# Optimization experiments

Measured on AMD Instinct MI355X. Metric: run time of the kernel, lower is better.

## Reference

```python
import jax, jax.numpy as jnp
import numpy as np
from math import sqrt

B, L, S = 8, 1024, 1000
D_MODEL, D_LLM, H, E = 1024, 4096, 16, 64  # d_keys = d_model // n_heads = 64


def setup_inputs() -> dict:
    key = jax.random.key(0)
    ks = jax.random.split(key, 11)
    s = 0.02
    return {
        "target_embedding": jax.random.normal(ks[0], (B, L, D_MODEL), jnp.float32),
        "source_embedding": jax.random.normal(ks[1], (S, D_LLM), jnp.float32),
        "value_embedding": jax.random.normal(ks[2], (S, D_LLM), jnp.float32),
        "Wq": jax.random.normal(ks[3], (D_MODEL, H * E), jnp.float32) * s,
        "bq": jnp.zeros((H * E,), jnp.float32),
        "Wk": jax.random.normal(ks[4], (D_LLM, H * E), jnp.float32) * s,
        "bk": jnp.zeros((H * E,), jnp.float32),
        "Wv": jax.random.normal(ks[5], (D_LLM, H * E), jnp.float32) * s,
        "bv": jnp.zeros((H * E,), jnp.float32),
        "Wo": jax.random.normal(ks[6], (H * E, D_LLM), jnp.float32) * s,
        "bo": jnp.zeros((D_LLM,), jnp.float32),
    }


def reference(target_embedding, source_embedding, value_embedding,
              Wq, bq, Wk, bk, Wv, bv, Wo, bo):
    b, l, _ = target_embedding.shape
    # projections
    q = (target_embedding @ Wq + bq).reshape(b, l, H, E)          # (B,L,H,E)
    k = (source_embedding @ Wk + bk).reshape(-1, H, E)            # (S,H,E) shared across batch
    v = (value_embedding @ Wv + bv).reshape(-1, H, E)             # (S,H,E)
    scale = 1.0 / sqrt(E)
    scores = jnp.einsum('blhe,she->bhls', q, k) * scale           # (B,H,L,S)
    A = jax.nn.softmax(scores, axis=-1)                           # dropout is identity (eval)
    out = jnp.einsum('bhls,she->blhe', A, v).reshape(b, l, H * E)
    return out @ Wo + bo                                          # (B,L,d_llm)
```

## Files before the change

kernel.cpp:

```cpp
#include <hip/hip_runtime.h>
#include <hip/hip_bf16.h>
#include <math.h>

#define B_SZ 8
#define L_SZ 1024
#define S_SZ 1000
#define DM   1024
#define DL   4096
#define NH   16
#define EH   64
#define QK_SCALE 0.180336880f

typedef __bf16 bf16x8 __attribute__((ext_vector_type(8)));
typedef __bf16 bf16x4 __attribute__((ext_vector_type(4)));
typedef float  f32x4  __attribute__((ext_vector_type(4)));

__device__ __forceinline__ void async16(const void* g, void* l) {
    __builtin_amdgcn_global_load_lds(
        (const __attribute__((address_space(1))) void*)g,
        (__attribute__((address_space(3))) void*)l, 16, 0, 0);
}

__global__ __launch_bounds__(256) void cast_all_kernel(
    const float* __restrict__ target, const float* __restrict__ source,
    const float* __restrict__ value, __bf16* __restrict__ Tb,
    __bf16* __restrict__ Sb, __bf16* __restrict__ Vb)
{
    int bid = blockIdx.x;
    const float* in; __bf16* out; int i;
    if (bid < 8192)       { in = target; out = Tb; i = bid * 256 + threadIdx.x; }
    else if (bid < 12192) { in = source; out = Sb; i = (bid - 8192)  * 256 + threadIdx.x; }
    else                  { in = value;  out = Vb; i = (bid - 12192) * 256 + threadIdx.x; }
    float4 x = ((const float4*)in)[i];
    bf16x4 y;
    y.x = (__bf16)x.x; y.y = (__bf16)x.y;
    y.z = (__bf16)x.z; y.w = (__bf16)x.w;
    ((bf16x4*)out)[i] = y;
}

__global__ __launch_bounds__(256) void transpose_all_kernel(
    const float* __restrict__ Wq, const float* __restrict__ Wk,
    const float* __restrict__ Wv, const float* __restrict__ Wo,
    __bf16* __restrict__ WqT, __bf16* __restrict__ WkT,
    __bf16* __restrict__ WvT, __bf16* __restrict__ WoT)
{
    __shared__ float t[64][68];
    int bid = blockIdx.x;
    const float* W; __bf16* WT; int K, N, bx, by;
    if (bid < 256)       { W = Wq; WT = WqT; K = DM; N = DM; int u = bid;        bx = u & 15; by = u >> 4; }
    else if (bid < 1280) { W = Wk; WT = WkT; K = DL; N = DM; int u = bid - 256;  bx = u & 15; by = u >> 4; }
    else if (bid < 2304) { W = Wv; WT = WvT; K = DL; N = DM; int u = bid - 1280; bx = u & 15; by = u >> 4; }
    else                 { W = Wo; WT = WoT; K = DM; N = DL; int u = bid - 2304; bx = u & 63; by = u >> 6; }
    const int k0 = by * 64, n0 = bx * 64;
    const int tx = threadIdx.x & 15, ty = threadIdx.x >> 4;

#pragma unroll
    for (int tt = 0; tt < 4; ++tt) {
        int r = ty + 16 * tt;
        float4 x = *(const float4*)&W[(size_t)(k0 + r) * N + n0 + 4 * tx];
        *(float4*)&t[r][4 * tx] = x;
    }
    __syncthreads();
#pragma unroll
    for (int tt = 0; tt < 4; ++tt) {
        int n = ty + 16 * tt;
        bf16x4 y;
        y.x = (__bf16)t[4 * tx + 0][n];
        y.y = (__bf16)t[4 * tx + 1][n];
        y.z = (__bf16)t[4 * tx + 2][n];
        y.w = (__bf16)t[4 * tx + 3][n];
        *(bf16x4*)&WT[(size_t)(n0 + n) * K + k0 + 4 * tx] = y;
    }
}

template <int OMODE>
__device__ __forceinline__ void gemm_body(
    const __bf16* __restrict__ A, int lda,
    const __bf16* __restrict__ BT, int ldb,
    const float* __restrict__ bias, void* __restrict__ Cv,
    int M, int N, int Kext, int bx, int by, float oscale,
    __bf16* As, __bf16* Bs)
{
    const int tid  = threadIdx.x;
    const int lane = tid & 63;
    const int wave = tid >> 6;
    const int wr   = wave >> 1;
    const int wc   = wave & 1;
    const int m0   = by * 128;
    const int n0   = bx * 128;
    const int lm   = lane & 15;
    const int lq   = lane >> 4;

    f32x4 acc[4][4];
#pragma unroll
    for (int i = 0; i < 4; ++i)
#pragma unroll
        for (int j = 0; j < 4; ++j)
            acc[i][j] = (f32x4){0.f, 0.f, 0.f, 0.f};

    for (int k0 = 0; k0 < Kext; k0 += 32) {
#pragma unroll
        for (int t = 0; t < 2; ++t) {
            int chunk = t * 256 + tid;
            int r     = chunk >> 2;
            int koff  = (chunk & 3) * 8;
            int gm = m0 + r; if (gm >= M) gm = M - 1;
            async16(A  + (size_t)gm * lda + k0 + koff, (char*)As + chunk * 16);
            int gn = n0 + r;
            async16(BT + (size_t)gn * ldb + k0 + koff, (char*)Bs + chunk * 16);
        }
        __syncthreads();

        bf16x8 af[4], bf_[4];
#pragma unroll
        for (int i = 0; i < 4; ++i) {
            af[i]  = *(const bf16x8*)&As[(wr * 64 + i * 16 + lm) * 32 + lq * 8];
            bf_[i] = *(const bf16x8*)&Bs[(wc * 64 + i * 16 + lm) * 32 + lq * 8];
        }
#pragma unroll
        for (int i = 0; i < 4; ++i)
#pragma unroll
            for (int j = 0; j < 4; ++j)
                acc[i][j] = __builtin_amdgcn_mfma_f32_16x16x32_bf16(
                    af[i], bf_[j], acc[i][j], 0, 0, 0);
        __syncthreads();
    }

#pragma unroll
    for (int i = 0; i < 4; ++i) {
        int gm0 = m0 + wr * 64 + i * 16 + lq * 4;
#pragma unroll
        for (int j = 0; j < 4; ++j) {
            int gn = n0 + wc * 64 + j * 16 + lm;
            float bv = (OMODE == 0) ? bias[gn] : 0.f;
#pragma unroll
            for (int r = 0; r < 4; ++r) {
                int gm = gm0 + r;
                if (gm < M) {
                    if (OMODE == 0)
                        ((__bf16*)Cv)[(size_t)gm * N + gn] =
                            (__bf16)((acc[i][j][r] + bv) * oscale);
                    else
                        ((float*)Cv)[(size_t)gm * N + gn] = acc[i][j][r];
                }
            }
        }
    }
}

__global__ __launch_bounds__(256) void qkv_fused_kernel(
    const __bf16* __restrict__ Tb, const __bf16* __restrict__ Sb,
    const __bf16* __restrict__ Vb,
    const __bf16* __restrict__ WqT, const __bf16* __restrict__ WkT,
    const __bf16* __restrict__ WvT,
    const float* __restrict__ bq,
    __bf16* __restrict__ qb, float* __restrict__ kpart, float* __restrict__ vpart)
{
    __shared__ __bf16 As[128 * 32];
    __shared__ __bf16 Bs[128 * 32];
    int bid = blockIdx.x;
    if (bid < 512) {
        int proj = bid >> 8;
        int u  = bid & 255;
        int ks = u >> 6;
        int v  = u & 63;
        const __bf16* Aop = (proj ? Vb : Sb) + ks * 1024;
        const __bf16* Bop = (proj ? WvT : WkT) + ks * 1024;
        float* Cp = (proj ? vpart : kpart) + (size_t)ks * 1024000;
        gemm_body<2>(Aop, DL, Bop, DL, nullptr, Cp, S_SZ, DM, 1024,
                     v & 7, v >> 3, 1.f, As, Bs);
    } else {
        int u = bid - 512;
        gemm_body<0>(Tb, DM, WqT, DM, bq, qb, B_SZ * L_SZ, DM, DM,
                     u & 7, u >> 3, QK_SCALE, As, Bs);
    }
}

__global__ __launch_bounds__(256) void combine_kv_kernel(
    const float* __restrict__ kpart, const float* __restrict__ vpart,
    const float* __restrict__ bk, const float* __restrict__ bv,
    __bf16* __restrict__ kb, __bf16* __restrict__ vtb)
{
    __shared__ float t[64][68];
    const int bid = blockIdx.x, tid = threadIdx.x;
    if (bid < 1000) {
        int e4 = bid * 256 + tid;
        int col = (e4 & 255) * 4;
        float4 s = *(const float4*)&bk[col];
#pragma unroll
        for (int j = 0; j < 4; ++j) {
            float4 pp = *(const float4*)&kpart[(size_t)j * 1024000 + (size_t)e4 * 4];
            s.x += pp.x; s.y += pp.y; s.z += pp.z; s.w += pp.w;
        }
        bf16x4 y;
        y.x = (__bf16)s.x; y.y = (__bf16)s.y;
        y.z = (__bf16)s.z; y.w = (__bf16)s.w;
        ((bf16x4*)kb)[e4] = y;
    } else {
        int u = bid - 1000;
        int d0 = (u & 15) * 64, s0 = (u >> 4) * 64;
#pragma unroll
        for (int tt = 0; tt < 4; ++tt) {
            int idx = tt * 256 + tid;
            int r = idx >> 4, c4 = idx & 15;
            float4 s = {0.f, 0.f, 0.f, 0.f};
            if (s0 + r < S_SZ) {
                s = *(const float4*)&bv[d0 + c4 * 4];
#pragma unroll
                for (int j = 0; j < 4; ++j) {
                    float4 pp = *(const float4*)&vpart[(size_t)j * 1024000
                                + (size_t)(s0 + r) * 1024 + d0 + c4 * 4];
                    s.x += pp.x; s.y += pp.y; s.z += pp.z; s.w += pp.w;
                }
            }
            *(float4*)&t[r][c4 * 4] = s;
        }
        __syncthreads();
#pragma unroll
        for (int tt = 0; tt < 2; ++tt) {
            int idx = tt * 256 + tid;
            int d = idx >> 3, ch = idx & 7;
            bf16x8 o;
#pragma unroll
            for (int j = 0; j < 8; ++j) o[j] = (__bf16)t[ch * 8 + j][d];
            *(bf16x8*)&vtb[(size_t)(d0 + d) * 1024 + s0 + ch * 8] = o;
        }
    }
}

__global__ __launch_bounds__(512, 2) void gemm_o8_kernel(
    const __bf16* __restrict__ A, const __bf16* __restrict__ BT,
    const float* __restrict__ bias, float* __restrict__ C)
{
    __shared__ __bf16 sA[3][256 * 32];
    __shared__ __bf16 sB[3][256 * 32];
    const int tid  = threadIdx.x;
    const int lane = tid & 63, wave = tid >> 6;
    const int wr = wave >> 2, wc = wave & 3;
    const int lm = lane & 15, lq = lane >> 4;
    const int K = 1024, NT = 32;

    int bid = blockIdx.x;
    bid = (bid & 7) * 64 + (bid >> 3);
    const int bx = bid & 15, by = bid >> 4;
    const int m0 = by * 256, n0 = bx * 256;

    f32x4 acc[8][4];
#pragma unroll
    for (int i = 0; i < 8; ++i)
#pragma unroll
        for (int j = 0; j < 4; ++j)
            acc[i][j] = (f32x4){0.f, 0.f, 0.f, 0.f};

    auto stage = [&](int slot, int t) {
        const int k0 = t * 32;
#pragma unroll
        for (int i = 0; i < 2; ++i) {
            int cc = i * 512 + tid;
            int r  = cc >> 2;
            int sg = (cc & 3) ^ ((r >> 1) & 3);
            async16(A  + (size_t)(m0 + r) * K + k0 + sg * 8,
                    (char*)sA[slot] + cc * 16);
            async16(BT + (size_t)(n0 + r) * K + k0 + sg * 8,
                    (char*)sB[slot] + cc * 16);
        }
    };

    stage(0, 0);
    stage(1, 1);
    asm volatile("s_waitcnt vmcnt(4)" ::: "memory");
    __builtin_amdgcn_s_barrier();
    __builtin_amdgcn_sched_barrier(0);

    int sl = 0;
    for (int t = 0; t < NT; ++t) {
        if (t + 2 < NT) {
            int s2 = sl + 2; if (s2 >= 3) s2 -= 3;
            stage(s2, t + 2);
        }
        bf16x8 fb[4], fa[8];
#pragma unroll
        for (int ni = 0; ni < 4; ++ni) {
            int rr = wc * 64 + ni * 16 + lm;
            fb[ni] = *(const bf16x8*)((const char*)sB[sl]
                     + rr * 64 + ((lq ^ ((rr >> 1) & 3)) * 16));
        }
#pragma unroll
        for (int mi = 0; mi < 4; ++mi) {
            int rr = wr * 128 + mi * 16 + lm;
            fa[mi] = *(const bf16x8*)((const char*)sA[sl]
                     + rr * 64 + ((lq ^ ((rr >> 1) & 3)) * 16));
        }
        __builtin_amdgcn_sched_barrier(0);
#pragma unroll
        for (int mi = 4; mi < 8; ++mi) {
            int rr = wr * 128 + mi * 16 + lm;
            fa[mi] = *(const bf16x8*)((const char*)sA[sl]
                     + rr * 64 + ((lq ^ ((rr >> 1) & 3)) * 16));
        }
        asm volatile("s_waitcnt lgkmcnt(4)" ::: "memory");
        __builtin_amdgcn_sched_barrier(0);
        __builtin_amdgcn_s_setprio(1);
#pragma unroll
        for (int mi = 0; mi < 4; ++mi)
#pragma unroll
            for (int ni = 0; ni < 4; ++ni)
                acc[mi][ni] = __builtin_amdgcn_mfma_f32_16x16x32_bf16(
                    fa[mi], fb[ni], acc[mi][ni], 0, 0, 0);
        __builtin_amdgcn_s_setprio(0);
        asm volatile("s_waitcnt lgkmcnt(0)" ::: "memory");
        __builtin_amdgcn_sched_barrier(0);
        __builtin_amdgcn_s_setprio(1);
#pragma unroll
        for (int mi = 4; mi < 8; ++mi)
#pragma unroll
            for (int ni = 0; ni < 4; ++ni)
                acc[mi][ni] = __builtin_amdgcn_mfma_f32_16x16x32_bf16(
                    fa[mi], fb[ni], acc[mi][ni], 0, 0, 0);
        __builtin_amdgcn_s_setprio(0);
        if (t + 2 < NT)
            asm volatile("s_waitcnt vmcnt(4)" ::: "memory");
        else
            asm volatile("s_waitcnt vmcnt(0)" ::: "memory");
        __builtin_amdgcn_s_barrier();
        __builtin_amdgcn_sched_barrier(0);
        if (++sl == 3) sl = 0;
    }

#pragma unroll
    for (int mi = 0; mi < 8; ++mi) {
        int gm0 = m0 + wr * 128 + mi * 16 + lq * 4;
#pragma unroll
        for (int ni = 0; ni < 4; ++ni) {
            int gn = n0 + wc * 64 + ni * 16 + lm;
            float bv = bias[gn];
#pragma unroll
            for (int r = 0; r < 4; ++r)
                C[(size_t)(gm0 + r) * 4096 + gn] = acc[mi][ni][r] + bv;
        }
    }
}

__global__ __launch_bounds__(256) void attn_mfma_kernel(
    const __bf16* __restrict__ q,
    const __bf16* __restrict__ k,
    const __bf16* __restrict__ vt,
    __bf16* __restrict__ o)
{
    __shared__ __bf16 Ks [2][64 * 64];
    __shared__ __bf16 Vts[2][64 * 64];
    __shared__ __bf16 Ps [4][32 * 72];

    const int tid  = threadIdx.x;
    const int lane = tid & 63;
    const int wave = tid >> 6;
    const int lm   = lane & 15;
    const int lq   = lane >> 4;
    const int bh = blockIdx.y;
    const int b  = bh >> 4;
    const int h  = bh & 15;
    const int l0 = blockIdx.x * 128;
    const int row0 = b * L_SZ + l0 + wave * 32;

    bf16x8 qf[2][2];
#pragma unroll
    for (int mt = 0; mt < 2; ++mt)
#pragma unroll
        for (int ks = 0; ks < 2; ++ks)
            qf[mt][ks] = *(const bf16x8*)&q[(size_t)(row0 + mt * 16 + lm) * DM
                                           + h * 64 + ks * 32 + lq * 8];

    f32x4 oa[2][4];
    f32x4 lacc[2];
    float m_run[2][4];
#pragma unroll
    for (int mt = 0; mt < 2; ++mt) {
        lacc[mt] = (f32x4){0.f, 0.f, 0.f, 0.f};
#pragma unroll
        for (int r = 0; r < 4; ++r) m_run[mt][r] = -1e30f;
#pragma unroll
        for (int et = 0; et < 4; ++et) oa[mt][et] = (f32x4){0.f, 0.f, 0.f, 0.f};
    }

    bf16x8 vones;
#pragma unroll
    for (int j = 0; j < 8; ++j) vones[j] = (__bf16)1.0f;

    auto stage = [&](int bi, int s0v) {
#pragma unroll
        for (int t = 0; t < 2; ++t) {
            int cc = t * 256 + tid;
            int r = cc >> 3, segL = cc & 7;
            int segG = segL ^ (r & 7);
            int sg = s0v + r; if (sg >= S_SZ) sg = S_SZ - 1;
            async16(k  + (size_t)sg * DM + h * 64 + segG * 8,
                    (char*)Ks[bi] + cc * 16);
            async16(vt + (size_t)(h * 64 + r) * 1024 + s0v + segG * 8,
                    (char*)Vts[bi] + cc * 16);
        }
    };

    stage(0, 0);
    int cur = 0;

    for (int s0 = 0; s0 < S_SZ; s0 += 64) {
        __syncthreads();
        if (s0 + 64 < S_SZ) stage(cur ^ 1, s0 + 64);

        f32x4 sc[2][4];
#pragma unroll
        for (int mt = 0; mt < 2; ++mt)
#pragma unroll
            for (int nt = 0; nt < 4; ++nt)
                sc[mt][nt] = (f32x4){0.f, 0.f, 0.f, 0.f};
#pragma unroll
        for (int ks = 0; ks < 2; ++ks)
#pragma unroll
            for (int nt = 0; nt < 4; ++nt) {
                bf16x8 bK = *(const bf16x8*)((const char*)Ks[cur]
                    + (nt * 16 + lm) * 128 + (((ks * 4 + lq) ^ (lm & 7)) * 16));
#pragma unroll
                for (int mt = 0; mt < 2; ++mt)
                    sc[mt][nt] = __builtin_amdgcn_mfma_f32_16x16x32_bf16(
                        qf[mt][ks], bK, sc[mt][nt], 0, 0, 0);
            }

        if (s0 + 64 > S_SZ) {
#pragma unroll
            for (int nt = 0; nt < 4; ++nt) {
                bool masked = (s0 + nt * 16 + lm >= S_SZ);
                if (masked)
#pragma unroll
                    for (int mt = 0; mt < 2; ++mt)
#pragma unroll
                        for (int r = 0; r < 4; ++r) sc[mt][nt][r] = -1e30f;
            }
        }

        float pm[2][4];
        bool ok = true;
#pragma unroll
        for (int mt = 0; mt < 2; ++mt)
#pragma unroll
            for (int r = 0; r < 4; ++r) {
                pm[mt][r] = fmaxf(fmaxf(sc[mt][0][r], sc[mt][1][r]),
                                  fmaxf(sc[mt][2][r], sc[mt][3][r]));
                ok = ok && (pm[mt][r] <= m_run[mt][r] + 8.f);
            }
        if (!__all((int)ok)) {
#pragma unroll
            for (int mt = 0; mt < 2; ++mt)
#pragma unroll
                for (int r = 0; r < 4; ++r) {
                    float mx = pm[mt][r];
#pragma unroll
                    for (int off = 1; off < 16; off <<= 1)
                        mx = fmaxf(mx, __shfl_xor(mx, off));
                    float mnew  = fmaxf(m_run[mt][r], mx);
                    float alpha = __builtin_amdgcn_exp2f(m_run[mt][r] - mnew);
                    m_run[mt][r] = mnew;
                    lacc[mt][r] *= alpha;
#pragma unroll
                    for (int et = 0; et < 4; ++et)
                        oa[mt][et][r] *= alpha;
                }
        }

#pragma unroll
        for (int mt = 0; mt < 2; ++mt)
#pragma unroll
            for (int r = 0; r < 4; ++r) {
                int prow = (mt * 16 + lq * 4 + r) * 72;
#pragma unroll
                for (int nt = 0; nt < 4; ++nt) {
                    float pv = __builtin_amdgcn_exp2f(sc[mt][nt][r] - m_run[mt][r]);
                    Ps[wave][prow + nt * 16 + lm] = (__bf16)pv;
                }
            }

        asm volatile("s_waitcnt lgkmcnt(0)" ::: "memory");

#pragma unroll
        for (int ks = 0; ks < 2; ++ks) {
            bf16x8 aP[2];
#pragma unroll
            for (int mt = 0; mt < 2; ++mt)
                aP[mt] = *(const bf16x8*)&Ps[wave][(mt * 16 + lm) * 72
                                                  + ks * 32 + lq * 8];
#pragma unroll
            for (int mt = 0; mt < 2; ++mt)
                lacc[mt] = __builtin_amdgcn_mfma_f32_16x16x32_bf16(
                    aP[mt], vones, lacc[mt], 0, 0, 0);
#pragma unroll
            for (int et = 0; et < 4; ++et) {
                bf16x8 bV = *(const bf16x8*)((const char*)Vts[cur]
                    + (et * 16 + lm) * 128 + (((ks * 4 + lq) ^ (lm & 7)) * 16));
#pragma unroll
                for (int mt = 0; mt < 2; ++mt)
                    oa[mt][et] = __builtin_amdgcn_mfma_f32_16x16x32_bf16(
                        aP[mt], bV, oa[mt][et], 0, 0, 0);
            }
        }
        cur ^= 1;
    }

#pragma unroll
    for (int mt = 0; mt < 2; ++mt)
#pragma unroll
        for (int r = 0; r < 4; ++r) {
            float inv = 1.f / lacc[mt][r];
            size_t rowi = (size_t)(row0 + mt * 16 + lq * 4 + r) * DM + h * 64;
#pragma unroll
            for (int et = 0; et < 4; ++et)
                o[rowi + et * 16 + lm] = (__bf16)(oa[mt][et][r] * inv);
        }
}

extern "C" void kernel_launch(void* const* d_in, const int* in_sizes, int n_in,
                              void* d_out, int out_size, void* d_ws, size_t ws_size,
                              hipStream_t stream)
{
    const float* target = (const float*)d_in[0];
    const float* source = (const float*)d_in[1];
    const float* value  = (const float*)d_in[2];
    const float* Wq = (const float*)d_in[3];
    const float* bq = (const float*)d_in[4];
    const float* Wk = (const float*)d_in[5];
    const float* bk = (const float*)d_in[6];
    const float* Wv = (const float*)d_in[7];
    const float* bv = (const float*)d_in[8];
    const float* Wo = (const float*)d_in[9];
    const float* bo = (const float*)d_in[10];
    float* out = (float*)d_out;

    char* p = (char*)d_ws;
    __bf16* Tb  = (__bf16*)(p);
    __bf16* Sb  = (__bf16*)(p + 16777216);
    __bf16* vtb = (__bf16*)(p + 16777216);
    __bf16* kb  = (__bf16*)(p + 24969216);
    __bf16* WqT = (__bf16*)(p + 29065216);
    __bf16* WoT = (__bf16*)(p + 31162368);
    char*   R   =           p + 39550976;
    __bf16* Vb  = (__bf16*)(R);
    __bf16* WvT = (__bf16*)(R + 8192000);
    __bf16* WkT = (__bf16*)(R + 16580608);
    __bf16* qb    = (__bf16*)d_out;
    float*  kpart = (float*)((char*)d_out + 16777216);
    float*  vpart = (float*)((char*)d_out + 33161216);
    __bf16* ab    = (__bf16*)(p);

    const dim3 blk(256);

    cast_all_kernel<<<16192, blk, 0, stream>>>(target, source, value, Tb, Sb, Vb);
    transpose_all_kernel<<<3328, blk, 0, stream>>>(Wq, Wk, Wv, Wo, WqT, WkT, WvT, WoT);
    qkv_fused_kernel<<<1024, blk, 0, stream>>>(Tb, Sb, Vb, WqT, WkT, WvT,
                                               bq, qb, kpart, vpart);
    combine_kv_kernel<<<1256, blk, 0, stream>>>(kpart, vpart, bk, bv, kb, vtb);
    attn_mfma_kernel<<<dim3(8, 128), blk, 0, stream>>>(qb, kb, vtb, ab);
    gemm_o8_kernel<<<512, 512, 0, stream>>>(ab, WoT, bo, out);
}
```

Baseline: 451.6 us.

## Unify projection GEMMs into 4-stage pipelined 256x256 kernel and merge prep kernels

```diff
diff --git a/kernel.cpp b/kernel.cpp
--- a/kernel.cpp
+++ b/kernel.cpp
@@ -10,6 +10,7 @@
 #define NH   16
 #define EH   64
 #define QK_SCALE 0.180336880f
+#define NTILES 32
 
 typedef __bf16 bf16x8 __attribute__((ext_vector_type(8)));
 typedef __bf16 bf16x4 __attribute__((ext_vector_type(4)));
@@ -21,31 +22,30 @@
         (__attribute__((address_space(3))) void*)l, 16, 0, 0);
 }
 
-__global__ __launch_bounds__(256) void cast_all_kernel(
+__global__ __launch_bounds__(256) void prep_kernel(
     const float* __restrict__ target, const float* __restrict__ source,
-    const float* __restrict__ value, __bf16* __restrict__ Tb,
-    __bf16* __restrict__ Sb, __bf16* __restrict__ Vb)
-{
-    int bid = blockIdx.x;
-    const float* in; __bf16* out; int i;
-    if (bid < 8192)       { in = target; out = Tb; i = bid * 256 + threadIdx.x; }
-    else if (bid < 12192) { in = source; out = Sb; i = (bid - 8192)  * 256 + threadIdx.x; }
-    else                  { in = value;  out = Vb; i = (bid - 12192) * 256 + threadIdx.x; }
-    float4 x = ((const float4*)in)[i];
-    bf16x4 y;
-    y.x = (__bf16)x.x; y.y = (__bf16)x.y;
-    y.z = (__bf16)x.z; y.w = (__bf16)x.w;
-    ((bf16x4*)out)[i] = y;
-}
-
-__global__ __launch_bounds__(256) void transpose_all_kernel(
+    const float* __restrict__ value,
     const float* __restrict__ Wq, const float* __restrict__ Wk,
     const float* __restrict__ Wv, const float* __restrict__ Wo,
+    __bf16* __restrict__ Tb, __bf16* __restrict__ Sb, __bf16* __restrict__ Vb,
     __bf16* __restrict__ WqT, __bf16* __restrict__ WkT,
     __bf16* __restrict__ WvT, __bf16* __restrict__ WoT)
 {
     __shared__ float t[64][68];
     int bid = blockIdx.x;
+    if (bid < 16192) {
+        const float* in; __bf16* out; int i;
+        if (bid < 8192)       { in = target; out = Tb; i = bid * 256 + threadIdx.x; }
+        else if (bid < 12192) { in = source; out = Sb; i = (bid - 8192)  * 256 + threadIdx.x; }
+        else                  { in = value;  out = Vb; i = (bid - 12192) * 256 + threadIdx.x; }
+        float4 x = ((const float4*)in)[i];
+        bf16x4 y;
+        y.x = (__bf16)x.x; y.y = (__bf16)x.y;
+        y.z = (__bf16)x.z; y.w = (__bf16)x.w;
+        ((bf16x4*)out)[i] = y;
+        return;
+    }
+    bid -= 16192;
     const float* W; __bf16* WT; int K, N, bx, by;
     if (bid < 256)       { W = Wq; WT = WqT; K = DM; N = DM; int u = bid;        bx = u & 15; by = u >> 4; }
     else if (bid < 1280) { W = Wk; WT = WkT; K = DL; N = DM; int u = bid - 256;  bx = u & 15; by = u >> 4; }
@@ -73,82 +73,124 @@
     }
 }
 
-template <int OMODE>
-__device__ __forceinline__ void gemm_body(
-    const __bf16* __restrict__ A, int lda,
-    const __bf16* __restrict__ BT, int ldb,
-    const float* __restrict__ bias, void* __restrict__ Cv,
-    int M, int N, int Kext, int bx, int by, float oscale,
-    __bf16* As, __bf16* Bs)
+__device__ __forceinline__ void pipe_body(
+    const __bf16* __restrict__ A, const __bf16* __restrict__ BT, int ld,
+    const float* __restrict__ bias, void* __restrict__ Cv, int ldc,
+    int M, int m0, int n0, float oscale, int omode,
+    __bf16 (*sA)[256 * 32], __bf16 (*sB)[256 * 32])
 {
     const int tid  = threadIdx.x;
-    const int lane = tid & 63;
-    const int wave = tid >> 6;
-    const int wr   = wave >> 1;
-    const int wc   = wave & 1;
-    const int m0   = by * 128;
-    const int n0   = bx * 128;
-    const int lm   = lane & 15;
-    const int lq   = lane >> 4;
-
-    f32x4 acc[4][4];
-#pragma unroll
-    for (int i = 0; i < 4; ++i)
+    const int lane = tid & 63, wave = tid >> 6;
+    const int wr = wave >> 2, wc = wave & 3;
+    const int lm = lane & 15, lq = lane >> 4;
+
+    f32x4 acc[8][4];
+#pragma unroll
+    for (int i = 0; i < 8; ++i)
 #pragma unroll
         for (int j = 0; j < 4; ++j)
             acc[i][j] = (f32x4){0.f, 0.f, 0.f, 0.f};
 
-    for (int k0 = 0; k0 < Kext; k0 += 32) {
-#pragma unroll
-        for (int t = 0; t < 2; ++t) {
-            int chunk = t * 256 + tid;
-            int r     = chunk >> 2;
-            int koff  = (chunk & 3) * 8;
+    auto stage = [&](int slot, int t) {
+        const int k0 = t * 32;
+#pragma unroll
+        for (int i = 0; i < 2; ++i) {
+            int cc = i * 512 + tid;
+            int r  = cc >> 2;
+            int sg = (cc & 3) ^ ((r >> 1) & 3);
             int gm = m0 + r; if (gm >= M) gm = M - 1;
-            async16(A  + (size_t)gm * lda + k0 + koff, (char*)As + chunk * 16);
-            int gn = n0 + r;
-            async16(BT + (size_t)gn * ldb + k0 + koff, (char*)Bs + chunk * 16);
-        }
-        __syncthreads();
-
-        bf16x8 af[4], bf_[4];
-#pragma unroll
-        for (int i = 0; i < 4; ++i) {
-            af[i]  = *(const bf16x8*)&As[(wr * 64 + i * 16 + lm) * 32 + lq * 8];
-            bf_[i] = *(const bf16x8*)&Bs[(wc * 64 + i * 16 + lm) * 32 + lq * 8];
-        }
-#pragma unroll
-        for (int i = 0; i < 4; ++i)
-#pragma unroll
-            for (int j = 0; j < 4; ++j)
-                acc[i][j] = __builtin_amdgcn_mfma_f32_16x16x32_bf16(
-                    af[i], bf_[j], acc[i][j], 0, 0, 0);
-        __syncthreads();
-    }
-
-#pragma unroll
-    for (int i = 0; i < 4; ++i) {
-        int gm0 = m0 + wr * 64 + i * 16 + lq * 4;
-#pragma unroll
-        for (int j = 0; j < 4; ++j) {
-            int gn = n0 + wc * 64 + j * 16 + lm;
-            float bv = (OMODE == 0) ? bias[gn] : 0.f;
+            async16(A  + (size_t)gm * ld + k0 + sg * 8,
+                    (char*)sA[slot] + cc * 16);
+            async16(BT + (size_t)(n0 + r) * ld + k0 + sg * 8,
+                    (char*)sB[slot] + cc * 16);
+        }
+    };
+
+    bf16x8 fa0[8], fb0[4], fa1[8], fb1[4];
+
+    auto read_frags = [&](int slot, bf16x8 (&fa)[8], bf16x8 (&fb)[4]) {
+#pragma unroll
+        for (int ni = 0; ni < 4; ++ni) {
+            int rr = wc * 64 + ni * 16 + lm;
+            fb[ni] = *(const bf16x8*)((const char*)sB[slot]
+                     + rr * 64 + ((lq ^ ((rr >> 1) & 3)) * 16));
+        }
+#pragma unroll
+        for (int mi = 0; mi < 8; ++mi) {
+            int rr = wr * 128 + mi * 16 + lm;
+            fa[mi] = *(const bf16x8*)((const char*)sA[slot]
+                     + rr * 64 + ((lq ^ ((rr >> 1) & 3)) * 16));
+        }
+    };
+
+    auto mfma_all = [&](bf16x8 (&fa)[8], bf16x8 (&fb)[4]) {
+        __builtin_amdgcn_s_setprio(1);
+#pragma unroll
+        for (int mi = 0; mi < 8; ++mi)
+#pragma unroll
+            for (int ni = 0; ni < 4; ++ni)
+                acc[mi][ni] = __builtin_amdgcn_mfma_f32_16x16x32_bf16(
+                    fa[mi], fb[ni], acc[mi][ni], 0, 0, 0);
+        __builtin_amdgcn_s_setprio(0);
+    };
+
+    stage(0, 0); stage(1, 1); stage(2, 2);
+    asm volatile("s_waitcnt vmcnt(4)" ::: "memory");
+    __builtin_amdgcn_s_barrier();
+    __builtin_amdgcn_sched_barrier(0);
+    read_frags(0, fa0, fb0);
+
+    for (int tt = 0; tt < NTILES; tt += 2) {
+        if (tt + 3 < NTILES) stage((tt + 3) & 3, tt + 3);
+        read_frags((tt + 1) & 3, fa1, fb1);
+        mfma_all(fa0, fb0);
+        if (tt + 3 < NTILES)
+            asm volatile("s_waitcnt vmcnt(4)" ::: "memory");
+        else
+            asm volatile("s_waitcnt vmcnt(0)" ::: "memory");
+        asm volatile("s_waitcnt lgkmcnt(0)" ::: "memory");
+        __builtin_amdgcn_sched_barrier(0);
+        __builtin_amdgcn_s_barrier();
+        __builtin_amdgcn_sched_barrier(0);
+
+        if (tt + 4 < NTILES) stage((tt + 4) & 3, tt + 4);
+        if (tt + 2 < NTILES) read_frags((tt + 2) & 3, fa0, fb0);
+        mfma_all(fa1, fb1);
+        if (tt + 2 < NTILES) {
+            if (tt + 4 < NTILES)
+                asm volatile("s_waitcnt vmcnt(4)" ::: "memory");
+            else
+                asm volatile("s_waitcnt vmcnt(0)" ::: "memory");
+            asm volatile("s_waitcnt lgkmcnt(0)" ::: "memory");
+            __builtin_amdgcn_sched_barrier(0);
+            __builtin_amdgcn_s_barrier();
+            __builtin_amdgcn_sched_barrier(0);
+        }
+    }
+
+#pragma unroll
+    for (int mi = 0; mi < 8; ++mi) {
+        int gm0 = m0 + wr * 128 + mi * 16 + lq * 4;
+#pragma unroll
+        for (int ni = 0; ni < 4; ++ni) {
+            int gn = n0 + wc * 64 + ni * 16 + lm;
+            float bv = (omode == 2) ? 0.f : bias[gn];
 #pragma unroll
             for (int r = 0; r < 4; ++r) {
                 int gm = gm0 + r;
                 if (gm < M) {
-                    if (OMODE == 0)
-                        ((__bf16*)Cv)[(size_t)gm * N + gn] =
-                            (__bf16)((acc[i][j][r] + bv) * oscale);
+                    float val = acc[mi][ni][r] + bv;
+                    if (omode == 0)
+                        ((__bf16*)Cv)[(size_t)gm * ldc + gn] = (__bf16)(val * oscale);
                     else
-                        ((float*)Cv)[(size_t)gm * N + gn] = acc[i][j][r];
+                        ((float*)Cv)[(size_t)gm * ldc + gn] = val;
                 }
             }
         }
     }
 }
 
-__global__ __launch_bounds__(256) void qkv_fused_kernel(
+__global__ __launch_bounds__(512, 2) void qkv_pipe_kernel(
     const __bf16* __restrict__ Tb, const __bf16* __restrict__ Sb,
     const __bf16* __restrict__ Vb,
     const __bf16* __restrict__ WqT, const __bf16* __restrict__ WkT,
@@ -156,24 +198,38 @@
     const float* __restrict__ bq,
     __bf16* __restrict__ qb, float* __restrict__ kpart, float* __restrict__ vpart)
 {
-    __shared__ __bf16 As[128 * 32];
-    __shared__ __bf16 Bs[128 * 32];
+    __shared__ __bf16 sA[4][256 * 32];
+    __shared__ __bf16 sB[4][256 * 32];
     int bid = blockIdx.x;
-    if (bid < 512) {
-        int proj = bid >> 8;
-        int u  = bid & 255;
-        int ks = u >> 6;
-        int v  = u & 63;
-        const __bf16* Aop = (proj ? Vb : Sb) + ks * 1024;
-        const __bf16* Bop = (proj ? WvT : WkT) + ks * 1024;
-        float* Cp = (proj ? vpart : kpart) + (size_t)ks * 1024000;
-        gemm_body<2>(Aop, DL, Bop, DL, nullptr, Cp, S_SZ, DM, 1024,
-                     v & 7, v >> 3, 1.f, As, Bs);
+    const __bf16 *A, *BT; const float* bias; void* Cv;
+    int ld, M, m0, n0, omode; float osc;
+    if (bid < 128) {
+        A = Tb; BT = WqT; bias = bq; Cv = qb; ld = DM; M = B_SZ * L_SZ;
+        m0 = (bid >> 2) * 256; n0 = (bid & 3) * 256; omode = 0; osc = QK_SCALE;
+    } else if (bid < 192) {
+        int u = bid - 128, ks = u >> 4, v = u & 15;
+        A = Sb + ks * 1024; BT = WkT + ks * 1024; bias = nullptr;
+        Cv = kpart + (size_t)ks * 1024000; ld = DL; M = S_SZ;
+        m0 = (v >> 2) * 256; n0 = (v & 3) * 256; omode = 2; osc = 1.f;
     } else {
-        int u = bid - 512;
-        gemm_body<0>(Tb, DM, WqT, DM, bq, qb, B_SZ * L_SZ, DM, DM,
-                     u & 7, u >> 3, QK_SCALE, As, Bs);
-    }
+        int u = bid - 192, ks = u >> 4, v = u & 15;
+        A = Vb + ks * 1024; BT = WvT + ks * 1024; bias = nullptr;
+        Cv = vpart + (size_t)ks * 1024000; ld = DL; M = S_SZ;
+        m0 = (v >> 2) * 256; n0 = (v & 3) * 256; omode = 2; osc = 1.f;
+    }
+    pipe_body(A, BT, ld, bias, Cv, DM, M, m0, n0, osc, omode, sA, sB);
+}
+
+__global__ __launch_bounds__(512, 2) void gemm_o_pipe_kernel(
+    const __bf16* __restrict__ ab, const __bf16* __restrict__ WoT,
+    const float* __restrict__ bo, float* __restrict__ out)
+{
+    __shared__ __bf16 sA[4][256 * 32];
+    __shared__ __bf16 sB[4][256 * 32];
+    int bid = blockIdx.x;
+    bid = (bid & 7) * 64 + (bid >> 3);
+    pipe_body(ab, WoT, DM, bo, out, DL, B_SZ * L_SZ,
+              (bid >> 4) * 256, (bid & 15) * 256, 1.f, 1, sA, sB);
 }
 
 __global__ __launch_bounds__(256) void combine_kv_kernel(
@@ -224,119 +280,6 @@
 #pragma unroll
             for (int j = 0; j < 8; ++j) o[j] = (__bf16)t[ch * 8 + j][d];
             *(bf16x8*)&vtb[(size_t)(d0 + d) * 1024 + s0 + ch * 8] = o;
-        }
-    }
-}
-
-__global__ __launch_bounds__(512, 2) void gemm_o8_kernel(
-    const __bf16* __restrict__ A, const __bf16* __restrict__ BT,
-    const float* __restrict__ bias, float* __restrict__ C)
-{
-    __shared__ __bf16 sA[3][256 * 32];
-    __shared__ __bf16 sB[3][256 * 32];
-    const int tid  = threadIdx.x;
-    const int lane = tid & 63, wave = tid >> 6;
-    const int wr = wave >> 2, wc = wave & 3;
-    const int lm = lane & 15, lq = lane >> 4;
-    const int K = 1024, NT = 32;
-
-    int bid = blockIdx.x;
-    bid = (bid & 7) * 64 + (bid >> 3);
-    const int bx = bid & 15, by = bid >> 4;
-    const int m0 = by * 256, n0 = bx * 256;
-
-    f32x4 acc[8][4];
-#pragma unroll
-    for (int i = 0; i < 8; ++i)
-#pragma unroll
-        for (int j = 0; j < 4; ++j)
-            acc[i][j] = (f32x4){0.f, 0.f, 0.f, 0.f};
-
-    auto stage = [&](int slot, int t) {
-        const int k0 = t * 32;
-#pragma unroll
-        for (int i = 0; i < 2; ++i) {
-            int cc = i * 512 + tid;
-            int r  = cc >> 2;
-            int sg = (cc & 3) ^ ((r >> 1) & 3);
-            async16(A  + (size_t)(m0 + r) * K + k0 + sg * 8,
-                    (char*)sA[slot] + cc * 16);
-            async16(BT + (size_t)(n0 + r) * K + k0 + sg * 8,
-                    (char*)sB[slot] + cc * 16);
-        }
-    };
-
-    stage(0, 0);
-    stage(1, 1);
-    asm volatile("s_waitcnt vmcnt(4)" ::: "memory");
-    __builtin_amdgcn_s_barrier();
-    __builtin_amdgcn_sched_barrier(0);
-
-    int sl = 0;
-    for (int t = 0; t < NT; ++t) {
-        if (t + 2 < NT) {
-            int s2 = sl + 2; if (s2 >= 3) s2 -= 3;
-            stage(s2, t + 2);
-        }
-        bf16x8 fb[4], fa[8];
-#pragma unroll
-        for (int ni = 0; ni < 4; ++ni) {
-            int rr = wc * 64 + ni * 16 + lm;
-            fb[ni] = *(const bf16x8*)((const char*)sB[sl]
-                     + rr * 64 + ((lq ^ ((rr >> 1) & 3)) * 16));
-        }
-#pragma unroll
-        for (int mi = 0; mi < 4; ++mi) {
-            int rr = wr * 128 + mi * 16 + lm;
-            fa[mi] = *(const bf16x8*)((const char*)sA[sl]
-                     + rr * 64 + ((lq ^ ((rr >> 1) & 3)) * 16));
-        }
-        __builtin_amdgcn_sched_barrier(0);
-#pragma unroll
-        for (int mi = 4; mi < 8; ++mi) {
-            int rr = wr * 128 + mi * 16 + lm;
-            fa[mi] = *(const bf16x8*)((const char*)sA[sl]
-                     + rr * 64 + ((lq ^ ((rr >> 1) & 3)) * 16));
-        }
-        asm volatile("s_waitcnt lgkmcnt(4)" ::: "memory");
-        __builtin_amdgcn_sched_barrier(0);
-        __builtin_amdgcn_s_setprio(1);
-#pragma unroll
-        for (int mi = 0; mi < 4; ++mi)
-#pragma unroll
-            for (int ni = 0; ni < 4; ++ni)
-                acc[mi][ni] = __builtin_amdgcn_mfma_f32_16x16x32_bf16(
-                    fa[mi], fb[ni], acc[mi][ni], 0, 0, 0);
-        __builtin_amdgcn_s_setprio(0);
-        asm volatile("s_waitcnt lgkmcnt(0)" ::: "memory");
-        __builtin_amdgcn_sched_barrier(0);
-        __builtin_amdgcn_s_setprio(1);
-#pragma unroll
-        for (int mi = 4; mi < 8; ++mi)
-#pragma unroll
-            for (int ni = 0; ni < 4; ++ni)
-                acc[mi][ni] = __builtin_amdgcn_mfma_f32_16x16x32_bf16(
-                    fa[mi], fb[ni], acc[mi][ni], 0, 0, 0);
-        __builtin_amdgcn_s_setprio(0);
-        if (t + 2 < NT)
-            asm volatile("s_waitcnt vmcnt(4)" ::: "memory");
-        else
-            asm volatile("s_waitcnt vmcnt(0)" ::: "memory");
-        __builtin_amdgcn_s_barrier();
-        __builtin_amdgcn_sched_barrier(0);
-        if (++sl == 3) sl = 0;
-    }
-
-#pragma unroll
-    for (int mi = 0; mi < 8; ++mi) {
-        int gm0 = m0 + wr * 128 + mi * 16 + lq * 4;
-#pragma unroll
-        for (int ni = 0; ni < 4; ++ni) {
-            int gn = n0 + wc * 64 + ni * 16 + lm;
-            float bv = bias[gn];
-#pragma unroll
-            for (int r = 0; r < 4; ++r)
-                C[(size_t)(gm0 + r) * 4096 + gn] = acc[mi][ni][r] + bv;
         }
     }
 }
@@ -549,13 +492,11 @@
     float*  vpart = (float*)((char*)d_out + 33161216);
     __bf16* ab    = (__bf16*)(p);
 
-    const dim3 blk(256);
-
-    cast_all_kernel<<<16192, blk, 0, stream>>>(target, source, value, Tb, Sb, Vb);
-    transpose_all_kernel<<<3328, blk, 0, stream>>>(Wq, Wk, Wv, Wo, WqT, WkT, WvT, WoT);
-    qkv_fused_kernel<<<1024, blk, 0, stream>>>(Tb, Sb, Vb, WqT, WkT, WvT,
-                                               bq, qb, kpart, vpart);
-    combine_kv_kernel<<<1256, blk, 0, stream>>>(kpart, vpart, bk, bv, kb, vtb);
-    attn_mfma_kernel<<<dim3(8, 128), blk, 0, stream>>>(qb, kb, vtb, ab);
-    gemm_o8_kernel<<<512, 512, 0, stream>>>(ab, WoT, bo, out);
-}
+    prep_kernel<<<19520, 256, 0, stream>>>(target, source, value, Wq, Wk, Wv, Wo,
+                                           Tb, Sb, Vb, WqT, WkT, WvT, WoT);
+    qkv_pipe_kernel<<<256, 512, 0, stream>>>(Tb, Sb, Vb, WqT, WkT, WvT,
+                                             bq, qb, kpart, vpart);
+    combine_kv_kernel<<<1256, 256, 0, stream>>>(kpart, vpart, bk, bv, kb, vtb);
+    attn_mfma_kernel<<<dim3(8, 128), 256, 0, stream>>>(qb, kb, vtb, ab);
+    gemm_o_pipe_kernel<<<512, 512, 0, stream>>>(ab, WoT, bo, out);
+}
```

Result: no change. 459.5 us (+1.8%).
